# Optimization experiments

Hardware: AMD Instinct MI355X
Metric: run time of the kernel (lower is better)

Reference implementation:

```python
import jax, jax.numpy as jnp
import numpy as np

B, H, S, D = 2, 12, 2048, 64

def setup_inputs() -> dict:
    key = jax.random.key(0)
    kq, kk, kv = jax.random.split(key, 3)
    Q = jax.random.normal(kq, (B, H, S, D), dtype=jnp.float32)
    K = jax.random.normal(kk, (B, H, S, D), dtype=jnp.float32)
    V = jax.random.normal(kv, (B, H, S, D), dtype=jnp.float32)
    return {"Q": Q, "K": K, "V": V}

def reference(Q, K, V):
    # NOTE: original code scales by sqrt(Q.shape[-2]) (the sequence length),
    # not the head dim — reproduced faithfully.
    scale = 1.0 / np.sqrt(Q.shape[-2]).astype(np.float32)
    scores = jnp.einsum('bhqd,bhkd->bhqk', Q, K) * scale  # [B,H,S,S]
    attn = jax.nn.softmax(scores, axis=-1)
    context = jnp.einsum('bhqk,bhkd->bhqd', attn, V)      # [B,H,S,D]
    # torch .squeeze(-1) only removes the last dim if it is size 1; D=64 so no-op
    return context
```

## Files before the change

### kernel.cpp

```cpp
#include <hip/hip_runtime.h>
#include <hip/hip_bf16.h>
#include <math.h>
#include <stdint.h>

#define BATCH 2
#define NH 12
#define SEQ 2048
#define HD 64
#define TQ 64
#define TK 64
#define NHEADS (BATCH*NH)
#define NIT (SEQ / TK)

typedef short bf16x8 __attribute__((ext_vector_type(8)));
typedef float f32x4 __attribute__((ext_vector_type(4)));
typedef float f32x16 __attribute__((ext_vector_type(16)));
typedef unsigned short us8_t __attribute__((ext_vector_type(8)));

#if __has_builtin(__builtin_amdgcn_exp2f)
#define EXP2F(x) __builtin_amdgcn_exp2f(x)
#else
#define EXP2F(x) exp2f(x)
#endif

static __device__ __forceinline__ unsigned short f2bf(float f) {
    unsigned int u = __float_as_uint(f);
    u += 0x7fffu + ((u >> 16) & 1u);
    return (unsigned short)(u >> 16);
}

static __device__ __forceinline__ unsigned int pack2bf(float a, float b) {
    __hip_bfloat162 v = __float22bfloat162_rn(float2{a, b});
    return *(unsigned int*)&v;
}

static __device__ __forceinline__ void async_cp16(const void* g, void* l) {
    __builtin_amdgcn_global_load_lds(
        (const __attribute__((address_space(1))) void*)g,
        (__attribute__((address_space(3))) void*)(uintptr_t)l,
        16, 0, 0);
}

__global__ __launch_bounds__(256)
void prep_qkv(const float* __restrict__ Q, const float* __restrict__ K,
              const float* __restrict__ V,
              unsigned short* __restrict__ Qb, unsigned short* __restrict__ Kb,
              unsigned short* __restrict__ Vtb, float qs) {
    const int bh = blockIdx.x >> 5;
    const int s0 = (blockIdx.x & 31) * 64;
    const int tid = threadIdx.x;
    const size_t off = ((size_t)bh * SEQ + s0) * HD;

    #pragma unroll
    for (int i = 0; i < 2; ++i) {
        size_t e0 = off + (size_t)(tid + 256 * i) * 8;
        float4 a = *(const float4*)&Q[e0];
        float4 b = *(const float4*)&Q[e0 + 4];
        us8_t rq = { f2bf(a.x*qs), f2bf(a.y*qs), f2bf(a.z*qs), f2bf(a.w*qs),
                     f2bf(b.x*qs), f2bf(b.y*qs), f2bf(b.z*qs), f2bf(b.w*qs) };
        *(us8_t*)&Qb[e0] = rq;
        float4 c = *(const float4*)&K[e0];
        float4 d = *(const float4*)&K[e0 + 4];
        us8_t rk = { f2bf(c.x), f2bf(c.y), f2bf(c.z), f2bf(c.w),
                     f2bf(d.x), f2bf(d.y), f2bf(d.z), f2bf(d.w) };
        *(us8_t*)&Kb[e0] = rk;
    }

    const float* Vsrc = V + off;
    unsigned short* Vdst = Vtb + (size_t)bh * HD * SEQ;
    const int n  = tid & 63;
    const int cg = tid >> 6;
    #pragma unroll
    for (int i = 0; i < 4; ++i) {
        int c4 = (cg + 4 * i) * 4;
        float4 v = *(const float4*)&Vsrc[(size_t)n * HD + c4];
        Vdst[(size_t)(c4 + 0) * SEQ + s0 + n] = f2bf(v.x);
        Vdst[(size_t)(c4 + 1) * SEQ + s0 + n] = f2bf(v.y);
        Vdst[(size_t)(c4 + 2) * SEQ + s0 + n] = f2bf(v.z);
        Vdst[(size_t)(c4 + 3) * SEQ + s0 + n] = f2bf(v.w);
    }
}

__global__ __launch_bounds__(256)
void fa_main(const unsigned short* __restrict__ Qb,
             const unsigned short* __restrict__ Kb,
             const unsigned short* __restrict__ Vtb,
             float* __restrict__ O) {
    const int x  = blockIdx.x & 7;
    const int t  = blockIdx.x >> 3;
    const int bh = x + 8 * (t % 3);
    const int qt = t / 3;
    const int q0 = qt * TQ;

    __shared__ unsigned short Ksh[2][TK * HD];
    __shared__ unsigned short Vsh[2][HD * TK];
    __shared__ unsigned short Ps[TQ * TK];
    __shared__ float Lsum[TQ];
    __shared__ float Linv[TQ];

    const int tid  = threadIdx.x;
    const int w    = tid >> 6;
    const int mt   = w >> 1;
    const int nt   = w & 1;
    const int lane = tid & 63;
    const int l31  = lane & 31;
    const int hi   = lane >> 5;
    const int l7   = lane & 7;
    const int r8   = lane >> 3;
    const int c8   = lane & 7;

    const unsigned short* Qh = Qb  + ((size_t)bh * SEQ + q0) * HD;
    const unsigned short* Kh = Kb  + (size_t)bh * SEQ * HD;
    const unsigned short* Vh = Vtb + (size_t)bh * HD * SEQ;

    {
        const int R = w * 16;
        async_cp16(Qh + (size_t)(R     + r8) * HD + (c8 ^ r8) * 8, &Ksh[1][ R      * HD]);
        async_cp16(Qh + (size_t)(R + 8 + r8) * HD + (c8 ^ r8) * 8, &Ksh[1][(R + 8) * HD]);
        async_cp16(Kh + (size_t)(R     + r8) * HD + (c8 ^ r8) * 8, &Ksh[0][ R      * HD]);
        async_cp16(Kh + (size_t)(R + 8 + r8) * HD + (c8 ^ r8) * 8, &Ksh[0][(R + 8) * HD]);
        async_cp16(Vh + (size_t)(R     + r8) * SEQ + (c8 ^ r8) * 8, &Vsh[0][ R      * HD]);
        async_cp16(Vh + (size_t)(R + 8 + r8) * SEQ + (c8 ^ r8) * 8, &Vsh[0][(R + 8) * HD]);
    }
    __syncthreads();

    bf16x8 qf[4];
    #pragma unroll
    for (int s = 0; s < 4; ++s)
        qf[s] = *(const bf16x8*)&Ksh[1][(mt*32 + l31) * HD + (((s*2 + hi) ^ l7) * 8)];
    __syncthreads();

    f32x16 o[2];
    o[0] = (f32x16)(0.f);
    o[1] = (f32x16)(0.f);
    float lsum = 0.f;

    for (int it = 0; it < NIT; ++it) {
        const int cur = it & 1;
        if (it + 1 < NIT) {
            const int nb  = cur ^ 1;
            const int kv0 = (it + 1) * TK;
            const int R   = w * 16;
            async_cp16(Kh + (size_t)(kv0 + R     + r8) * HD  + (c8 ^ r8) * 8, &Ksh[nb][ R      * HD]);
            async_cp16(Kh + (size_t)(kv0 + R + 8 + r8) * HD  + (c8 ^ r8) * 8, &Ksh[nb][(R + 8) * HD]);
            async_cp16(Vh + (size_t)(R     + r8) * SEQ + kv0 + (c8 ^ r8) * 8, &Vsh[nb][ R      * HD]);
            async_cp16(Vh + (size_t)(R + 8 + r8) * SEQ + kv0 + (c8 ^ r8) * 8, &Vsh[nb][(R + 8) * HD]);
        }
        const unsigned short* Ks = Ksh[cur];
        const unsigned short* Vs = Vsh[cur];

        f32x16 sc = (f32x16)(0.f);
        #pragma unroll
        for (int s = 0; s < 4; ++s) {
            bf16x8 kf = *(const bf16x8*)&Ks[(nt*32 + l31) * HD + (((s*2 + hi) ^ l7) * 8)];
            sc = __builtin_amdgcn_mfma_f32_32x32x16_bf16(kf, qf[s], sc, 0, 0, 0);
        }

        float e[16];
        #pragma unroll
        for (int r = 0; r < 16; ++r) e[r] = EXP2F(sc[r]);
        #pragma unroll
        for (int r = 0; r < 16; ++r) lsum += e[r];
        #pragma unroll
        for (int g = 0; g < 4; ++g) {
            const int m = mt*32 + l31;
            const int ch = nt*4 + g;
            uint2 pk = { pack2bf(e[4*g+0], e[4*g+1]), pack2bf(e[4*g+2], e[4*g+3]) };
            *(uint2*)&Ps[m * TK + ((ch ^ (m & 7)) * 8) + hi * 4] = pk;
        }

        bf16x8 pf[2];
        #pragma unroll
        for (int ks = 0; ks < 2; ++ks) {
            const int m = mt*32 + l31;
            const int ch = nt*4 + ks*2 + hi;
            pf[ks] = *(const bf16x8*)&Ps[m * TK + ((ch ^ (m & 7)) * 8)];
        }
        #pragma unroll
        for (int dt = 0; dt < 2; ++dt) {
            const int d = dt*32 + l31;
            #pragma unroll
            for (int ks = 0; ks < 2; ++ks) {
                const int ch = nt*4 + ks*2 + hi;
                bf16x8 vf = *(const bf16x8*)&Vs[d * HD + ((ch ^ l7) * 8)];
                o[dt] = __builtin_amdgcn_mfma_f32_32x32x16_bf16(pf[ks], vf, o[dt], 0, 0, 0);
            }
        }

        __syncthreads();
    }

    lsum += __shfl_xor(lsum, 32, 64);
    float* ORed = (float*)Ksh;

    if (nt == 1) {
        if (lane < 32) Lsum[mt*32 + lane] = lsum;
        #pragma unroll
        for (int dt = 0; dt < 2; ++dt) {
            const int d = dt*32 + l31;
            #pragma unroll
            for (int g = 0; g < 4; ++g) {
                const int m0 = mt*32 + 8*g + 4*hi;
                const int ph = (m0 >> 2) ^ (d & 15);
                float4 v = { o[dt][4*g+0], o[dt][4*g+1], o[dt][4*g+2], o[dt][4*g+3] };
                *(float4*)&ORed[d * 64 + ph * 4] = v;
            }
        }
    }
    __syncthreads();

    if (nt == 0) {
        float ltot = lsum + Lsum[mt*32 + l31];
        if (lane < 32) Linv[mt*32 + lane] = 1.0f / ltot;
        float* Oh = O + ((size_t)bh * SEQ + q0) * HD;
        #pragma unroll
        for (int dt = 0; dt < 2; ++dt) {
            const int d = dt*32 + l31;
            #pragma unroll
            for (int g = 0; g < 4; ++g) {
                const int m0 = mt*32 + 8*g + 4*hi;
                const int ph = (m0 >> 2) ^ (d & 15);
                float4 part = *(const float4*)&ORed[d * 64 + ph * 4];
                float4 inv4 = *(const float4*)&Linv[m0];
                const float* pp = (const float*)&part;
                const float* ii = (const float*)&inv4;
                #pragma unroll
                for (int j = 0; j < 4; ++j)
                    Oh[(size_t)(m0 + j) * HD + d] = (o[dt][4*g+j] + pp[j]) * ii[j];
            }
        }
    }
}

#define PAD 8
#define LSTR (HD + PAD)

__global__ __launch_bounds__(256)
void fa_fwd_fb(const float* __restrict__ Q, const float* __restrict__ K,
               const float* __restrict__ V, float* __restrict__ O) {
    const int x  = blockIdx.x & 7;
    const int t  = blockIdx.x >> 3;
    const int bh = x + 8 * (t % 3);
    const int qt = t / 3;
    const int q0 = qt * TQ;
    const long base = (long)bh * SEQ * HD;

    __shared__ unsigned short Qs[TQ][LSTR];
    __shared__ unsigned short Ks2[TK][LSTR];
    __shared__ unsigned short Vt[HD][TK + PAD];
    __shared__ unsigned short Ps2[4][16][LSTR];

    const int tid  = threadIdx.x;
    const int wave = tid >> 6;
    const int lane = tid & 63;
    const int col  = lane & 15;
    const int quad = lane >> 4;
    const int m0   = wave * 16;

    #pragma unroll
    for (int i = 0; i < 4; ++i) {
        int idx = tid + 256 * i;
        int row = idx >> 4;
        int c4  = (idx & 15) * 4;
        float4 v = *(const float4*)&Q[base + (long)(q0 + row) * HD + c4];
        ushort4 b = { f2bf(v.x), f2bf(v.y), f2bf(v.z), f2bf(v.w) };
        *(ushort4*)&Qs[row][c4] = b;
    }
    __syncthreads();

    bf16x8 aq0 = *(const bf16x8*)&Qs[m0 + col][quad * 8];
    bf16x8 aq1 = *(const bf16x8*)&Qs[m0 + col][32 + quad * 8];

    f32x4 o0 = {0.f,0.f,0.f,0.f}, o1 = o0, o2 = o0, o3 = o0;
    float l[4] = {0.f, 0.f, 0.f, 0.f};
    const float scale = 0.022097086912079608f;

    for (int kv0 = 0; kv0 < SEQ; kv0 += TK) {
        __syncthreads();
        #pragma unroll
        for (int i = 0; i < 4; ++i) {
            int idx = tid + 256 * i;
            int row = idx >> 4;
            int c4  = (idx & 15) * 4;
            float4 kv = *(const float4*)&K[base + (long)(kv0 + row) * HD + c4];
            ushort4 kb = { f2bf(kv.x), f2bf(kv.y), f2bf(kv.z), f2bf(kv.w) };
            *(ushort4*)&Ks2[row][c4] = kb;
            float4 vv = *(const float4*)&V[base + (long)(kv0 + row) * HD + c4];
            Vt[c4 + 0][row] = f2bf(vv.x);
            Vt[c4 + 1][row] = f2bf(vv.y);
            Vt[c4 + 2][row] = f2bf(vv.z);
            Vt[c4 + 3][row] = f2bf(vv.w);
        }
        __syncthreads();

        f32x4 sc[4];
        #pragma unroll
        for (int n = 0; n < 4; ++n) {
            bf16x8 b0 = *(const bf16x8*)&Ks2[n * 16 + col][quad * 8];
            bf16x8 b1 = *(const bf16x8*)&Ks2[n * 16 + col][32 + quad * 8];
            f32x4 acc = {0.f,0.f,0.f,0.f};
            acc = __builtin_amdgcn_mfma_f32_16x16x32_bf16(aq0, b0, acc, 0, 0, 0);
            acc = __builtin_amdgcn_mfma_f32_16x16x32_bf16(aq1, b1, acc, 0, 0, 0);
            sc[n] = acc;
        }

        float tsum[4] = {0.f, 0.f, 0.f, 0.f};
        #pragma unroll
        for (int n = 0; n < 4; ++n) {
            #pragma unroll
            for (int r = 0; r < 4; ++r) {
                float p = __expf(sc[n][r] * scale);
                tsum[r] += p;
                Ps2[wave][quad * 4 + r][n * 16 + col] = f2bf(p);
            }
        }
        #pragma unroll
        for (int off = 1; off < 16; off <<= 1) {
            #pragma unroll
            for (int r = 0; r < 4; ++r) tsum[r] += __shfl_xor(tsum[r], off, 64);
        }
        #pragma unroll
        for (int r = 0; r < 4; ++r) l[r] += tsum[r];

        bf16x8 ap0 = *(const bf16x8*)&Ps2[wave][col][quad * 8];
        bf16x8 ap1 = *(const bf16x8*)&Ps2[wave][col][32 + quad * 8];
        #pragma unroll
        for (int n = 0; n < 4; ++n) {
            bf16x8 b0 = *(const bf16x8*)&Vt[n * 16 + col][quad * 8];
            bf16x8 b1 = *(const bf16x8*)&Vt[n * 16 + col][32 + quad * 8];
            f32x4* op = (n == 0) ? &o0 : (n == 1) ? &o1 : (n == 2) ? &o2 : &o3;
            *op = __builtin_amdgcn_mfma_f32_16x16x32_bf16(ap0, b0, *op, 0, 0, 0);
            *op = __builtin_amdgcn_mfma_f32_16x16x32_bf16(ap1, b1, *op, 0, 0, 0);
        }
    }

    float inv[4];
    #pragma unroll
    for (int r = 0; r < 4; ++r) inv[r] = 1.0f / l[r];
    #pragma unroll
    for (int r = 0; r < 4; ++r) {
        long row = base + (long)(q0 + m0 + quad * 4 + r) * HD;
        O[row +  0 + col] = o0[r] * inv[r];
        O[row + 16 + col] = o1[r] * inv[r];
        O[row + 32 + col] = o2[r] * inv[r];
        O[row + 48 + col] = o3[r] * inv[r];
    }
}

extern "C" void kernel_launch(void* const* d_in, const int* in_sizes, int n_in,
                              void* d_out, int out_size, void* d_ws, size_t ws_size,
                              hipStream_t stream) {
    const float* Q = (const float*)d_in[0];
    const float* K = (const float*)d_in[1];
    const float* V = (const float*)d_in[2];
    float* O = (float*)d_out;

    const size_t tensorElems = (size_t)NHEADS * SEQ * HD;
    const size_t need = 3 * tensorElems * sizeof(unsigned short);

    if (ws_size >= need) {
        unsigned short* Qb  = (unsigned short*)d_ws;
        unsigned short* Kb  = Qb + tensorElems;
        unsigned short* Vtb = Kb + tensorElems;
        const float qs = (float)(1.4426950408889634 / sqrt(2048.0));
        prep_qkv<<<dim3(NHEADS * (SEQ / 64)), dim3(256), 0, stream>>>(Q, K, V, Qb, Kb, Vtb, qs);
        fa_main<<<dim3(NHEADS * (SEQ / TQ)), dim3(256), 0, stream>>>(Qb, Kb, Vtb, O);
    } else {
        fa_fwd_fb<<<dim3(NHEADS * (SEQ / TQ)), dim3(256), 0, stream>>>(Q, K, V, O);
    }
}
```

Before: 126.5 us.

## Fuse Q conversion into attention kernel and transpose V through LDS in prep

Q is no longer converted to bf16 in the prep kernel. The attention kernel now reads fp32 Q directly, scales it and packs it to bf16 in shared memory, which removes a global write and read of Qb. The prep kernel transposes V through an LDS tile, so it can write 16-byte vectors instead of scattered 2-byte stores. LDS tiles also switch to a new pair-row XOR swizzle with precomputed per-lane offsets, and the exp/sum/pack loop is restructured.

```diff
diff --git a/kernel.cpp b/kernel.cpp
--- a/kernel.cpp
+++ b/kernel.cpp
@@ -15,6 +15,7 @@
 typedef short bf16x8 __attribute__((ext_vector_type(8)));
 typedef float f32x4 __attribute__((ext_vector_type(4)));
 typedef float f32x16 __attribute__((ext_vector_type(16)));
+typedef unsigned short us4_t __attribute__((ext_vector_type(4)));
 typedef unsigned short us8_t __attribute__((ext_vector_type(8)));
 
 #if __has_builtin(__builtin_amdgcn_exp2f)
@@ -41,62 +42,65 @@
         16, 0, 0);
 }
 
+static __device__ __forceinline__ int tile_off(int r, int c) {
+    int rp  = r >> 1;
+    int pos = (((r & 1) << 3) | c) ^ (rp & 15);
+    return rp * 128 + pos * 8;
+}
+
 __global__ __launch_bounds__(256)
-void prep_qkv(const float* __restrict__ Q, const float* __restrict__ K,
-              const float* __restrict__ V,
-              unsigned short* __restrict__ Qb, unsigned short* __restrict__ Kb,
-              unsigned short* __restrict__ Vtb, float qs) {
+void prep_kv(const float* __restrict__ K, const float* __restrict__ V,
+             unsigned short* __restrict__ Kb, unsigned short* __restrict__ Vtb) {
+    __shared__ unsigned short T[64][66];
     const int bh = blockIdx.x >> 5;
     const int s0 = (blockIdx.x & 31) * 64;
     const int tid = threadIdx.x;
     const size_t off = ((size_t)bh * SEQ + s0) * HD;
 
     #pragma unroll
-    for (int i = 0; i < 2; ++i) {
-        size_t e0 = off + (size_t)(tid + 256 * i) * 8;
-        float4 a = *(const float4*)&Q[e0];
-        float4 b = *(const float4*)&Q[e0 + 4];
-        us8_t rq = { f2bf(a.x*qs), f2bf(a.y*qs), f2bf(a.z*qs), f2bf(a.w*qs),
-                     f2bf(b.x*qs), f2bf(b.y*qs), f2bf(b.z*qs), f2bf(b.w*qs) };
-        *(us8_t*)&Qb[e0] = rq;
-        float4 c = *(const float4*)&K[e0];
-        float4 d = *(const float4*)&K[e0 + 4];
-        us8_t rk = { f2bf(c.x), f2bf(c.y), f2bf(c.z), f2bf(c.w),
-                     f2bf(d.x), f2bf(d.y), f2bf(d.z), f2bf(d.w) };
-        *(us8_t*)&Kb[e0] = rk;
-    }
-
-    const float* Vsrc = V + off;
+    for (int u = 0; u < 4; ++u) {
+        int idx = u * 1024 + tid * 4;
+        float4 a = *(const float4*)&K[off + idx];
+        us4_t r4 = { f2bf(a.x), f2bf(a.y), f2bf(a.z), f2bf(a.w) };
+        *(us4_t*)&Kb[off + idx] = r4;
+    }
+    #pragma unroll
+    for (int u = 0; u < 4; ++u) {
+        int idx = u * 1024 + tid * 4;
+        int r = idx >> 6, col = idx & 63;
+        float4 a = *(const float4*)&V[off + idx];
+        *(unsigned int*)&T[r][col]     = pack2bf(a.x, a.y);
+        *(unsigned int*)&T[r][col + 2] = pack2bf(a.z, a.w);
+    }
+    __syncthreads();
     unsigned short* Vdst = Vtb + (size_t)bh * HD * SEQ;
-    const int n  = tid & 63;
-    const int cg = tid >> 6;
-    #pragma unroll
-    for (int i = 0; i < 4; ++i) {
-        int c4 = (cg + 4 * i) * 4;
-        float4 v = *(const float4*)&Vsrc[(size_t)n * HD + c4];
-        Vdst[(size_t)(c4 + 0) * SEQ + s0 + n] = f2bf(v.x);
-        Vdst[(size_t)(c4 + 1) * SEQ + s0 + n] = f2bf(v.y);
-        Vdst[(size_t)(c4 + 2) * SEQ + s0 + n] = f2bf(v.z);
-        Vdst[(size_t)(c4 + 3) * SEQ + s0 + n] = f2bf(v.w);
+    const int g = tid & 7, dd = tid >> 3;
+    #pragma unroll
+    for (int h = 0; h < 2; ++h) {
+        int d = dd + 32 * h;
+        us8_t r8;
+        #pragma unroll
+        for (int j = 0; j < 8; ++j) r8[j] = T[g * 8 + j][d];
+        *(us8_t*)&Vdst[(size_t)d * SEQ + s0 + g * 8] = r8;
     }
 }
 
 __global__ __launch_bounds__(256)
-void fa_main(const unsigned short* __restrict__ Qb,
+void fa_main(const float* __restrict__ Q,
              const unsigned short* __restrict__ Kb,
              const unsigned short* __restrict__ Vtb,
-             float* __restrict__ O) {
+             float* __restrict__ O, float qs) {
     const int x  = blockIdx.x & 7;
     const int t  = blockIdx.x >> 3;
     const int bh = x + 8 * (t % 3);
     const int qt = t / 3;
     const int q0 = qt * TQ;
 
-    __shared__ unsigned short Ksh[2][TK * HD];
-    __shared__ unsigned short Vsh[2][HD * TK];
-    __shared__ unsigned short Ps[TQ * TK];
-    __shared__ float Lsum[TQ];
-    __shared__ float Linv[TQ];
+    __shared__ __align__(16) unsigned short KtS[2][4096];
+    __shared__ __align__(16) unsigned short VtS[2][4096];
+    __shared__ __align__(16) unsigned short Ps[4096];
+    __shared__ float Lsum[64];
+    __shared__ float Linv[64];
 
     const int tid  = threadIdx.x;
     const int w    = tid >> 6;
@@ -105,30 +109,58 @@
     const int lane = tid & 63;
     const int l31  = lane & 31;
     const int hi   = lane >> 5;
-    const int l7   = lane & 7;
-    const int r8   = lane >> 3;
-    const int c8   = lane & 7;
-
-    const unsigned short* Qh = Qb  + ((size_t)bh * SEQ + q0) * HD;
+
+    const float*          Qh = Q   + ((size_t)bh * SEQ + q0) * HD;
     const unsigned short* Kh = Kb  + (size_t)bh * SEQ * HD;
     const unsigned short* Vh = Vtb + (size_t)bh * HD * SEQ;
 
-    {
-        const int R = w * 16;
-        async_cp16(Qh + (size_t)(R     + r8) * HD + (c8 ^ r8) * 8, &Ksh[1][ R      * HD]);
-        async_cp16(Qh + (size_t)(R + 8 + r8) * HD + (c8 ^ r8) * 8, &Ksh[1][(R + 8) * HD]);
-        async_cp16(Kh + (size_t)(R     + r8) * HD + (c8 ^ r8) * 8, &Ksh[0][ R      * HD]);
-        async_cp16(Kh + (size_t)(R + 8 + r8) * HD + (c8 ^ r8) * 8, &Ksh[0][(R + 8) * HD]);
-        async_cp16(Vh + (size_t)(R     + r8) * SEQ + (c8 ^ r8) * 8, &Vsh[0][ R      * HD]);
-        async_cp16(Vh + (size_t)(R + 8 + r8) * SEQ + (c8 ^ r8) * 8, &Vsh[0][(R + 8) * HD]);
+    int rS[2], cS[2];
+    #pragma unroll
+    for (int i = 0; i < 2; ++i) {
+        int rp = w * 8 + 4 * i + (lane >> 4);
+        int lc = (lane & 15) ^ (rp & 15);
+        rS[i] = 2 * rp + (lc >> 3);
+        cS[i] = lc & 7;
+    }
+    const int dst0 = (w * 8 + 0) * 128, dst1 = (w * 8 + 4) * 128;
+    const size_t kG0 = (size_t)rS[0] * HD  + cS[0] * 8;
+    const size_t kG1 = (size_t)rS[1] * HD  + cS[1] * 8;
+    const size_t vG0 = (size_t)rS[0] * SEQ + cS[0] * 8;
+    const size_t vG1 = (size_t)rS[1] * SEQ + cS[1] * 8;
+
+    async_cp16(Kh + kG0, &KtS[0][dst0]);
+    async_cp16(Kh + kG1, &KtS[0][dst1]);
+    async_cp16(Vh + vG0, &VtS[0][dst0]);
+    async_cp16(Vh + vG1, &VtS[0][dst1]);
+    #pragma unroll
+    for (int u = 0; u < 4; ++u) {
+        int idx = u * 1024 + tid * 4;
+        int r = idx >> 6, col = idx & 63;
+        float4 a = *(const float4*)&Qh[idx];
+        uint2 pk = { pack2bf(a.x * qs, a.y * qs), pack2bf(a.z * qs, a.w * qs) };
+        *(uint2*)&Ps[tile_off(r, col >> 3) + (col & 7)] = pk;
     }
     __syncthreads();
 
     bf16x8 qf[4];
     #pragma unroll
     for (int s = 0; s < 4; ++s)
-        qf[s] = *(const bf16x8*)&Ksh[1][(mt*32 + l31) * HD + (((s*2 + hi) ^ l7) * 8)];
-    __syncthreads();
+        qf[s] = *(const bf16x8*)&Ps[tile_off(mt * 32 + l31, s * 2 + hi)];
+    __syncthreads();
+
+    const int m = mt * 32 + l31;
+    int kOffL[4], vOffL[2][2], pW[4], pR[2];
+    #pragma unroll
+    for (int s = 0; s < 4; ++s) kOffL[s] = tile_off(nt * 32 + l31, s * 2 + hi);
+    #pragma unroll
+    for (int dt = 0; dt < 2; ++dt)
+        #pragma unroll
+        for (int ks = 0; ks < 2; ++ks)
+            vOffL[dt][ks] = tile_off(dt * 32 + l31, nt * 4 + ks * 2 + hi);
+    #pragma unroll
+    for (int g = 0; g < 4; ++g) pW[g] = tile_off(m, nt * 4 + g) + hi * 4;
+    #pragma unroll
+    for (int ks = 0; ks < 2; ++ks) pR[ks] = tile_off(m, nt * 4 + ks * 2 + hi);
 
     f32x16 o[2];
     o[0] = (f32x16)(0.f);
@@ -138,69 +170,58 @@
     for (int it = 0; it < NIT; ++it) {
         const int cur = it & 1;
         if (it + 1 < NIT) {
-            const int nb  = cur ^ 1;
-            const int kv0 = (it + 1) * TK;
-            const int R   = w * 16;
-            async_cp16(Kh + (size_t)(kv0 + R     + r8) * HD  + (c8 ^ r8) * 8, &Ksh[nb][ R      * HD]);
-            async_cp16(Kh + (size_t)(kv0 + R + 8 + r8) * HD  + (c8 ^ r8) * 8, &Ksh[nb][(R + 8) * HD]);
-            async_cp16(Vh + (size_t)(R     + r8) * SEQ + kv0 + (c8 ^ r8) * 8, &Vsh[nb][ R      * HD]);
-            async_cp16(Vh + (size_t)(R + 8 + r8) * SEQ + kv0 + (c8 ^ r8) * 8, &Vsh[nb][(R + 8) * HD]);
-        }
-        const unsigned short* Ks = Ksh[cur];
-        const unsigned short* Vs = Vsh[cur];
+            const int nb = cur ^ 1;
+            const size_t kv = (size_t)(it + 1) * TK;
+            async_cp16(Kh + kv * HD + kG0, &KtS[nb][dst0]);
+            async_cp16(Kh + kv * HD + kG1, &KtS[nb][dst1]);
+            async_cp16(Vh + kv + vG0,      &VtS[nb][dst0]);
+            async_cp16(Vh + kv + vG1,      &VtS[nb][dst1]);
+        }
+        const unsigned short* Ks = KtS[cur];
+        const unsigned short* Vs = VtS[cur];
 
         f32x16 sc = (f32x16)(0.f);
         #pragma unroll
         for (int s = 0; s < 4; ++s) {
-            bf16x8 kf = *(const bf16x8*)&Ks[(nt*32 + l31) * HD + (((s*2 + hi) ^ l7) * 8)];
+            bf16x8 kf = *(const bf16x8*)&Ks[kOffL[s]];
             sc = __builtin_amdgcn_mfma_f32_32x32x16_bf16(kf, qf[s], sc, 0, 0, 0);
         }
 
-        float e[16];
-        #pragma unroll
-        for (int r = 0; r < 16; ++r) e[r] = EXP2F(sc[r]);
-        #pragma unroll
-        for (int r = 0; r < 16; ++r) lsum += e[r];
         #pragma unroll
         for (int g = 0; g < 4; ++g) {
-            const int m = mt*32 + l31;
-            const int ch = nt*4 + g;
-            uint2 pk = { pack2bf(e[4*g+0], e[4*g+1]), pack2bf(e[4*g+2], e[4*g+3]) };
-            *(uint2*)&Ps[m * TK + ((ch ^ (m & 7)) * 8) + hi * 4] = pk;
-        }
-
-        bf16x8 pf[2];
-        #pragma unroll
-        for (int ks = 0; ks < 2; ++ks) {
-            const int m = mt*32 + l31;
-            const int ch = nt*4 + ks*2 + hi;
-            pf[ks] = *(const bf16x8*)&Ps[m * TK + ((ch ^ (m & 7)) * 8)];
-        }
+            float p0 = EXP2F(sc[4*g+0]);
+            float p1 = EXP2F(sc[4*g+1]);
+            float p2 = EXP2F(sc[4*g+2]);
+            float p3 = EXP2F(sc[4*g+3]);
+            lsum += (p0 + p1) + (p2 + p3);
+            uint2 pk = { pack2bf(p0, p1), pack2bf(p2, p3) };
+            *(uint2*)&Ps[pW[g]] = pk;
+        }
+
+        bf16x8 pf0 = *(const bf16x8*)&Ps[pR[0]];
+        bf16x8 pf1 = *(const bf16x8*)&Ps[pR[1]];
         #pragma unroll
         for (int dt = 0; dt < 2; ++dt) {
-            const int d = dt*32 + l31;
-            #pragma unroll
-            for (int ks = 0; ks < 2; ++ks) {
-                const int ch = nt*4 + ks*2 + hi;
-                bf16x8 vf = *(const bf16x8*)&Vs[d * HD + ((ch ^ l7) * 8)];
-                o[dt] = __builtin_amdgcn_mfma_f32_32x32x16_bf16(pf[ks], vf, o[dt], 0, 0, 0);
-            }
+            bf16x8 vf0 = *(const bf16x8*)&Vs[vOffL[dt][0]];
+            o[dt] = __builtin_amdgcn_mfma_f32_32x32x16_bf16(pf0, vf0, o[dt], 0, 0, 0);
+            bf16x8 vf1 = *(const bf16x8*)&Vs[vOffL[dt][1]];
+            o[dt] = __builtin_amdgcn_mfma_f32_32x32x16_bf16(pf1, vf1, o[dt], 0, 0, 0);
         }
 
         __syncthreads();
     }
 
     lsum += __shfl_xor(lsum, 32, 64);
-    float* ORed = (float*)Ksh;
+    float* ORed = (float*)&KtS[0][0];
 
     if (nt == 1) {
-        if (lane < 32) Lsum[mt*32 + lane] = lsum;
+        if (lane < 32) Lsum[mt * 32 + lane] = lsum;
         #pragma unroll
         for (int dt = 0; dt < 2; ++dt) {
-            const int d = dt*32 + l31;
+            const int d = dt * 32 + l31;
             #pragma unroll
             for (int g = 0; g < 4; ++g) {
-                const int m0 = mt*32 + 8*g + 4*hi;
+                const int m0 = mt * 32 + 8 * g + 4 * hi;
                 const int ph = (m0 >> 2) ^ (d & 15);
                 float4 v = { o[dt][4*g+0], o[dt][4*g+1], o[dt][4*g+2], o[dt][4*g+3] };
                 *(float4*)&ORed[d * 64 + ph * 4] = v;
@@ -210,15 +231,15 @@
     __syncthreads();
 
     if (nt == 0) {
-        float ltot = lsum + Lsum[mt*32 + l31];
-        if (lane < 32) Linv[mt*32 + lane] = 1.0f / ltot;
+        float ltot = lsum + Lsum[mt * 32 + l31];
+        if (lane < 32) Linv[mt * 32 + lane] = 1.0f / ltot;
         float* Oh = O + ((size_t)bh * SEQ + q0) * HD;
         #pragma unroll
         for (int dt = 0; dt < 2; ++dt) {
-            const int d = dt*32 + l31;
+            const int d = dt * 32 + l31;
             #pragma unroll
             for (int g = 0; g < 4; ++g) {
-                const int m0 = mt*32 + 8*g + 4*hi;
+                const int m0 = mt * 32 + 8 * g + 4 * hi;
                 const int ph = (m0 >> 2) ^ (d & 15);
                 float4 part = *(const float4*)&ORed[d * 64 + ph * 4];
                 float4 inv4 = *(const float4*)&Linv[m0];
@@ -356,15 +377,14 @@
     float* O = (float*)d_out;
 
     const size_t tensorElems = (size_t)NHEADS * SEQ * HD;
-    const size_t need = 3 * tensorElems * sizeof(unsigned short);
+    const size_t need = 2 * tensorElems * sizeof(unsigned short);
 
     if (ws_size >= need) {
-        unsigned short* Qb  = (unsigned short*)d_ws;
-        unsigned short* Kb  = Qb + tensorElems;
+        unsigned short* Kb  = (unsigned short*)d_ws;
         unsigned short* Vtb = Kb + tensorElems;
         const float qs = (float)(1.4426950408889634 / sqrt(2048.0));
-        prep_qkv<<<dim3(NHEADS * (SEQ / 64)), dim3(256), 0, stream>>>(Q, K, V, Qb, Kb, Vtb, qs);
-        fa_main<<<dim3(NHEADS * (SEQ / TQ)), dim3(256), 0, stream>>>(Qb, Kb, Vtb, O);
+        prep_kv<<<dim3(NHEADS * (SEQ / 64)), dim3(256), 0, stream>>>(K, V, Kb, Vtb);
+        fa_main<<<dim3(NHEADS * (SEQ / TQ)), dim3(256), 0, stream>>>(Q, Kb, Vtb, O, qs);
     } else {
         fa_fwd_fb<<<dim3(NHEADS * (SEQ / TQ)), dim3(256), 0, stream>>>(Q, K, V, O);
     }
```

After: 125.6 us. No clear change (-0.7%).
